# Optimization experiments

Measured on AMD Instinct MI355X. Metric: run time of the kernel, lower is better.

Reference implementation:

```python
import jax, jax.numpy as jnp
import numpy as np

D_MODEL = 1024
N_HEADS = 16
N_KV = 1          # MQA: the torch module only repeats xk_attn/sv, so n_kv must be 1 or n_heads
HEAD_DIM = 64     # d_model // total_n_heads
B = 1
L = 2048
SCALE = 1.0 / np.sqrt(HEAD_DIM)


def _rope(x, cos, sin):
    # x: [B, L, H, hd]; cos/sin: [L, hd//2]; pairs are consecutive elements (llama2.c style)
    xr, xi = x[..., 0::2], x[..., 1::2]
    c = cos[None, :, None, :]
    s = sin[None, :, None, :]
    out_r = xr * c - xi * s
    out_i = xr * s + xi * c
    return jnp.stack([out_r, out_i], axis=-1).reshape(x.shape)


def setup_inputs() -> dict:
    key = jax.random.key(0)
    ks = jax.random.split(key, 8)
    x = jax.random.normal(ks[0], (B, L, D_MODEL), dtype=jnp.float32)
    symbols = jax.random.normal(ks[1], (B, L, D_MODEL), dtype=jnp.float32)
    # standard RoPE frequencies
    inv_freq = 1.0 / (10000.0 ** (np.arange(0, HEAD_DIM, 2, dtype=np.float64) / HEAD_DIM))
    angles = np.outer(np.arange(L, dtype=np.float64), inv_freq)
    freqs_cos = jnp.asarray(np.cos(angles), dtype=jnp.float32)
    freqs_sin = jnp.asarray(np.sin(angles), dtype=jnp.float32)
    s = 0.02
    wq_attn = jax.random.normal(ks[2], (D_MODEL, N_HEADS * HEAD_DIM), dtype=jnp.float32) * s
    wk_attn = jax.random.normal(ks[3], (D_MODEL, N_KV * HEAD_DIM), dtype=jnp.float32) * s
    wq_rel = jax.random.normal(ks[4], (D_MODEL, N_HEADS * HEAD_DIM), dtype=jnp.float32) * s
    wk_rel = jax.random.normal(ks[5], (D_MODEL, N_KV * HEAD_DIM), dtype=jnp.float32) * s
    wv = jax.random.normal(ks[6], (D_MODEL, N_KV * HEAD_DIM), dtype=jnp.float32) * s
    wo = jax.random.normal(ks[7], (N_HEADS * HEAD_DIM, N_HEADS * HEAD_DIM), dtype=jnp.float32) * s
    return {"x": x, "symbols": symbols, "freqs_cos": freqs_cos, "freqs_sin": freqs_sin,
            "wq_attn": wq_attn, "wk_attn": wk_attn, "wq_rel": wq_rel, "wk_rel": wk_rel,
            "wv": wv, "wo": wo}


def reference(x, symbols, freqs_cos, freqs_sin, wq_attn, wk_attn, wq_rel, wk_rel, wv, wo):
    bsz, seqlen, _ = x.shape
    n_rep = N_HEADS // N_KV
    # projections
    xq_a = (x @ wq_attn).reshape(bsz, seqlen, N_HEADS, HEAD_DIM)
    xk_a = (x @ wk_attn).reshape(bsz, seqlen, N_KV, HEAD_DIM)
    xq_r = (x @ wq_rel).reshape(bsz, seqlen, N_HEADS, HEAD_DIM)
    xk_r = (x @ wk_rel).reshape(bsz, seqlen, N_KV, HEAD_DIM)
    sv = (symbols @ wv).reshape(bsz, seqlen, N_KV, HEAD_DIM)
    # RoPE only on attention q/k (matches torch code)
    xq_a = _rope(xq_a, freqs_cos, freqs_sin)
    xk_a = _rope(xk_a, freqs_cos, freqs_sin)
    # GQA/MQA head repetition of attn keys and symbol-values (NOT rel keys, per source)
    xk_a = jnp.repeat(xk_a, n_rep, axis=2)   # [B, L, H, hd]
    sv = jnp.repeat(sv, n_rep, axis=2)       # [B, L, H, hd]
    # attention scores with causal mask
    attn_scores = jnp.einsum('bihd,bjhd->bhij', xq_a, xk_a) * SCALE
    causal_bias = jnp.where(jnp.tril(jnp.ones((seqlen, seqlen), dtype=bool)),
                            jnp.float32(0.0), -jnp.inf)
    attn_scores = jax.nn.softmax(attn_scores + causal_bias, axis=-1)
    # relation scores: xk_r has N_KV=1 heads, broadcast against H query heads (identity activation)
    rel_scores = jnp.einsum('bihd,bjd->bhij', xq_r, xk_r[:, :, 0, :]) * SCALE
    rca_scores = attn_scores * rel_scores
    out = jnp.einsum('bhij,bjhd->bihd', rca_scores, sv)
    out = out.reshape(bsz, seqlen, N_HEADS * HEAD_DIM) @ wo
    return (out, attn_scores, rel_scores)
```

## Files before the change

kernel.cpp:

```cpp
#include <hip/hip_runtime.h>
#include <hip/hip_bf16.h>
#include <stdint.h>

#define LQ 2048
#define DM 1024
#define NH 16
#define HD 64
#define NPAIR 32
#define SCALE_F 0.125f

#define QROWS 16
__global__ __launch_bounds__(256) void k_proj_q(
    const float* __restrict__ x, const float* __restrict__ wqa, const float* __restrict__ wqr,
    const float* __restrict__ fcos, const float* __restrict__ fsin,
    float* __restrict__ Qa, float* __restrict__ Qr)
{
    __shared__ float xS[QROWS * DM];
    const int bid = blockIdx.x;
    const int i0 = (bid >> 2) * QROWS;
    const int m = (bid >> 1) & 1;
    const int half = bid & 1;
    const int tid = threadIdx.x;
    {
        const float4* src = (const float4*)(x + (size_t)i0 * DM);
        float4* dst4 = (float4*)xS;
        for (int t = tid; t < QROWS * DM / 4; t += 256) dst4[t] = src[t];
    }
    __syncthreads();
    const int q = half * 256 + tid;
    const float2* __restrict__ w2 = (const float2*)(m ? wqr : wqa);
    float ae[QROWS], ao[QROWS];
#pragma unroll
    for (int r = 0; r < QROWS; ++r) { ae[r] = 0.f; ao[r] = 0.f; }
    for (int k = 0; k < DM; k += 4) {
        float2 w0 = w2[(size_t)(k + 0) * (DM / 2) + q];
        float2 w1 = w2[(size_t)(k + 1) * (DM / 2) + q];
        float2 w2v = w2[(size_t)(k + 2) * (DM / 2) + q];
        float2 w3 = w2[(size_t)(k + 3) * (DM / 2) + q];
#pragma unroll
        for (int r = 0; r < QROWS; ++r) {
            float4 xv = *(const float4*)&xS[r * DM + k];
            ae[r] = fmaf(xv.x, w0.x, ae[r]);  ao[r] = fmaf(xv.x, w0.y, ao[r]);
            ae[r] = fmaf(xv.y, w1.x, ae[r]);  ao[r] = fmaf(xv.y, w1.y, ao[r]);
            ae[r] = fmaf(xv.z, w2v.x, ae[r]); ao[r] = fmaf(xv.z, w2v.y, ao[r]);
            ae[r] = fmaf(xv.w, w3.x, ae[r]);  ao[r] = fmaf(xv.w, w3.y, ao[r]);
        }
    }
    float* __restrict__ dst = m ? Qr : Qa;
    const int p = q & (NPAIR - 1);
#pragma unroll
    for (int r = 0; r < QROWS; ++r) {
        float oe = ae[r], oo = ao[r];
        if (m == 0) {
            float c = fcos[(i0 + r) * NPAIR + p];
            float s = fsin[(i0 + r) * NPAIR + p];
            oe = ae[r] * c - ao[r] * s;
            oo = ae[r] * s + ao[r] * c;
        }
        *(float2*)&dst[(size_t)(i0 + r) * DM + 2 * q] = make_float2(oe, oo);
    }
}

#define KVROWS 8
__global__ __launch_bounds__(128) void k_proj_kv(
    const float* __restrict__ x, const float* __restrict__ symbols,
    const float* __restrict__ wka, const float* __restrict__ wkr, const float* __restrict__ wv,
    const float* __restrict__ fcos, const float* __restrict__ fsin,
    float* __restrict__ Ka, float* __restrict__ Kr, float* __restrict__ SV)
{
    __shared__ float xS[KVROWS * DM], sS[KVROWS * DM];
    const int i0 = blockIdx.x * KVROWS;
    const int tid = threadIdx.x;
    {
        const float4* sx = (const float4*)(x + (size_t)i0 * DM);
        const float4* ss = (const float4*)(symbols + (size_t)i0 * DM);
        for (int t = tid; t < KVROWS * DM / 4; t += 128) {
            ((float4*)xS)[t] = sx[t];
            ((float4*)sS)[t] = ss[t];
        }
    }
    __syncthreads();
    if (tid >= 96) return;
    const int m = tid >> 5;
    const int p = tid & 31;
    const float2* __restrict__ w2 = (const float2*)(m == 0 ? wka : (m == 1 ? wkr : wv));
    const float* __restrict__ src = (m == 2) ? sS : xS;
    float ae[KVROWS], ao[KVROWS];
#pragma unroll
    for (int r = 0; r < KVROWS; ++r) { ae[r] = 0.f; ao[r] = 0.f; }
    for (int k = 0; k < DM; ++k) {
        float2 w = w2[k * 32 + p];
#pragma unroll
        for (int r = 0; r < KVROWS; ++r) {
            float xv = src[r * DM + k];
            ae[r] = fmaf(xv, w.x, ae[r]);
            ao[r] = fmaf(xv, w.y, ao[r]);
        }
    }
    float* __restrict__ dst = (m == 0 ? Ka : (m == 1 ? Kr : SV));
#pragma unroll
    for (int r = 0; r < KVROWS; ++r) {
        float oe = ae[r], oo = ao[r];
        if (m == 0) {
            float c = fcos[(i0 + r) * NPAIR + p];
            float s = fsin[(i0 + r) * NPAIR + p];
            oe = ae[r] * c - ao[r] * s;
            oo = ae[r] * s + ao[r] * c;
        }
        dst[(i0 + r) * HD + 2 * p] = oe;
        dst[(i0 + r) * HD + 2 * p + 1] = oo;
    }
}

__global__ __launch_bounds__(256) void k_rel(
    const float* __restrict__ Qr, const float* __restrict__ Kr, float* __restrict__ relout)
{
    __shared__ float QS[128 * 68];
    __shared__ float KS[64 * 68];
    const int j0 = blockIdx.x * 64, i0 = blockIdx.y * 128, h = blockIdx.z;
    const int tid = threadIdx.x;
    for (int t = tid; t < 128 * 16; t += 256) {
        int r = t >> 4, c4 = (t & 15) << 2;
        *(float4*)&QS[r * 68 + c4] = *(const float4*)&Qr[(size_t)(i0 + r) * DM + h * HD + c4];
    }
    for (int t = tid; t < 64 * 16; t += 256) {
        int r = t >> 4, c4 = (t & 15) << 2;
        *(float4*)&KS[r * 68 + c4] = *(const float4*)&Kr[(j0 + r) * HD + c4];
    }
    __syncthreads();
    const int ti = tid & 15, tj = tid >> 4;
    float acc[8][4] = {};
#pragma unroll 2
    for (int d = 0; d < HD; d += 4) {
        float4 kv[4];
#pragma unroll
        for (int b = 0; b < 4; ++b) kv[b] = *(const float4*)&KS[(tj * 4 + b) * 68 + d];
#pragma unroll
        for (int a = 0; a < 8; ++a) {
            float4 qv = *(const float4*)&QS[(ti + 16 * a) * 68 + d];
#pragma unroll
            for (int b = 0; b < 4; ++b) {
                acc[a][b] = fmaf(qv.x, kv[b].x, acc[a][b]);
                acc[a][b] = fmaf(qv.y, kv[b].y, acc[a][b]);
                acc[a][b] = fmaf(qv.z, kv[b].z, acc[a][b]);
                acc[a][b] = fmaf(qv.w, kv[b].w, acc[a][b]);
            }
        }
    }
#pragma unroll
    for (int a = 0; a < 8; ++a) {
        float4 w = make_float4(acc[a][0] * SCALE_F, acc[a][1] * SCALE_F,
                               acc[a][2] * SCALE_F, acc[a][3] * SCALE_F);
        *(float4*)&relout[(size_t)(h * LQ + i0 + ti + 16 * a) * LQ + j0 + tj * 4] = w;
    }
}

__global__ __launch_bounds__(256) void k_attn_fused(
    const float* __restrict__ Qa, const float* __restrict__ Ka, const float* __restrict__ SV,
    const float* __restrict__ relin, float* __restrict__ attnout, float* __restrict__ OutH)
{
    __shared__ float QS[64 * 68];
    __shared__ float KSbuf[64 * 68];
    __shared__ float SVS[64 * 68];
    const int bid = blockIdx.x;
    const int h = bid & 15;
    const int m = bid >> 4;
    const int it = (m < 16) ? m : 47 - m;
    const int i0 = it * 64;
    const int tid = threadIdx.x;
    for (int t = tid; t < 64 * 16; t += 256) {
        int r = t >> 4, c4 = (t & 15) << 2;
        *(float4*)&QS[r * 68 + c4] = *(const float4*)&Qa[(size_t)(i0 + r) * DM + h * HD + c4];
    }
    const int ti = tid & 15, tj = tid >> 4;
    float l_[4] = {0.f, 0.f, 0.f, 0.f};
    float oacc[4][4] = {};
    float* pS = KSbuf;
    for (int jt = 0; jt <= it; ++jt) {
        const int j0 = jt * 64;
        __syncthreads();
        for (int t = tid; t < 64 * 16; t += 256) {
            int r = t >> 4, c4 = (t & 15) << 2;
            *(float4*)&KSbuf[r * 68 + c4] = *(const float4*)&Ka[(j0 + r) * HD + c4];
            *(float4*)&SVS[r * 68 + c4]  = *(const float4*)&SV[(j0 + r) * HD + c4];
        }
        const int jb = j0 + tj * 4;
        float4 rv[4];
#pragma unroll
        for (int a = 0; a < 4; ++a)
            rv[a] = *(const float4*)&relin[(size_t)(h * LQ + i0 + ti + 16 * a) * LQ + jb];
        __syncthreads();
        float s[4][4] = {};
#pragma unroll 2
        for (int d = 0; d < HD; d += 4) {
            float4 kv[4];
#pragma unroll
            for (int b = 0; b < 4; ++b) kv[b] = *(const float4*)&KSbuf[(tj * 4 + b) * 68 + d];
#pragma unroll
            for (int a = 0; a < 4; ++a) {
                float4 qv = *(const float4*)&QS[(ti + 16 * a) * 68 + d];
#pragma unroll
                for (int b = 0; b < 4; ++b) {
                    s[a][b] = fmaf(qv.x, kv[b].x, s[a][b]);
                    s[a][b] = fmaf(qv.y, kv[b].y, s[a][b]);
                    s[a][b] = fmaf(qv.z, kv[b].z, s[a][b]);
                    s[a][b] = fmaf(qv.w, kv[b].w, s[a][b]);
                }
            }
        }
        __syncthreads();
#pragma unroll
        for (int a = 0; a < 4; ++a) {
            const int i = i0 + ti + 16 * a;
            const float* rl = (const float*)&rv[a];
            float e0 = (jb + 0 <= i) ? __expf(s[a][0] * SCALE_F) : 0.f;
            float e1 = (jb + 1 <= i) ? __expf(s[a][1] * SCALE_F) : 0.f;
            float e2 = (jb + 2 <= i) ? __expf(s[a][2] * SCALE_F) : 0.f;
            float e3 = (jb + 3 <= i) ? __expf(s[a][3] * SCALE_F) : 0.f;
            l_[a] += e0 + e1 + e2 + e3;
            *(float4*)&pS[(ti + 16 * a) * 68 + tj * 4] =
                make_float4(e0 * rl[0], e1 * rl[1], e2 * rl[2], e3 * rl[3]);
            *(float4*)&attnout[(size_t)(h * LQ + i) * LQ + jb] =
                make_float4(e0, e1, e2, e3);
        }
        __syncthreads();
#pragma unroll 2
        for (int g = 0; g < 64; g += 4) {
            float4 sv0 = *(const float4*)&SVS[(g + 0) * 68 + tj * 4];
            float4 sv1 = *(const float4*)&SVS[(g + 1) * 68 + tj * 4];
            float4 sv2 = *(const float4*)&SVS[(g + 2) * 68 + tj * 4];
            float4 sv3 = *(const float4*)&SVS[(g + 3) * 68 + tj * 4];
#pragma unroll
            for (int a = 0; a < 4; ++a) {
                float4 p4 = *(const float4*)&pS[(ti + 16 * a) * 68 + g];
                oacc[a][0] = fmaf(p4.x, sv0.x, oacc[a][0]);
                oacc[a][1] = fmaf(p4.x, sv0.y, oacc[a][1]);
                oacc[a][2] = fmaf(p4.x, sv0.z, oacc[a][2]);
                oacc[a][3] = fmaf(p4.x, sv0.w, oacc[a][3]);
                oacc[a][0] = fmaf(p4.y, sv1.x, oacc[a][0]);
                oacc[a][1] = fmaf(p4.y, sv1.y, oacc[a][1]);
                oacc[a][2] = fmaf(p4.y, sv1.z, oacc[a][2]);
                oacc[a][3] = fmaf(p4.y, sv1.w, oacc[a][3]);
                oacc[a][0] = fmaf(p4.z, sv2.x, oacc[a][0]);
                oacc[a][1] = fmaf(p4.z, sv2.y, oacc[a][1]);
                oacc[a][2] = fmaf(p4.z, sv2.z, oacc[a][2]);
                oacc[a][3] = fmaf(p4.z, sv2.w, oacc[a][3]);
                oacc[a][0] = fmaf(p4.w, sv3.x, oacc[a][0]);
                oacc[a][1] = fmaf(p4.w, sv3.y, oacc[a][1]);
                oacc[a][2] = fmaf(p4.w, sv3.z, oacc[a][2]);
                oacc[a][3] = fmaf(p4.w, sv3.w, oacc[a][3]);
            }
        }
    }
    __syncthreads();
    float* red = SVS;
#pragma unroll
    for (int a = 0; a < 4; ++a) red[(ti + 16 * a) * 17 + tj] = l_[a];
    __syncthreads();
    if (tid < 64) {
        float Ls = 0.f;
#pragma unroll
        for (int t = 0; t < 16; ++t) Ls += red[tid * 17 + t];
        red[tid * 17 + 16] = 1.0f / Ls;
    }
    __syncthreads();
#pragma unroll
    for (int a = 0; a < 4; ++a) {
        float inv = red[(ti + 16 * a) * 17 + 16];
        *(float4*)&OutH[(size_t)(i0 + ti + 16 * a) * DM + h * HD + tj * 4] =
            make_float4(oacc[a][0] * inv, oacc[a][1] * inv,
                        oacc[a][2] * inv, oacc[a][3] * inv);
    }
    const int lastc4 = (it + 1) * 16;
    for (int idx = tid; idx < 64 * (LQ / 4); idx += 256) {
        const int r = idx >> 9, c4 = idx & 511;
        float* p = &attnout[(size_t)(h * LQ + i0 + r) * LQ + (c4 << 2)];
        if (c4 < lastc4) {
            const float inv = red[r * 17 + 16];
            float4 v = *(const float4*)p;
            v.x *= inv; v.y *= inv; v.z *= inv; v.w *= inv;
            *(float4*)p = v;
        } else {
            *(float4*)p = make_float4(0.f, 0.f, 0.f, 0.f);
        }
    }
}

__global__ __launch_bounds__(256) void k_outproj(
    const float* __restrict__ OutH, const float* __restrict__ wo, float* __restrict__ outp)
{
    __shared__ float AS[64 * 68];
    __shared__ float BS[64 * 68];
    const int n0 = blockIdx.x * 64, i0 = blockIdx.y * 64;
    const int tid = threadIdx.x;
    const int ti = tid & 15, tj = tid >> 4;
    float acc[4][4] = {};
    for (int kt = 0; kt < DM / 64; ++kt) {
        const int k0 = kt * 64;
        __syncthreads();
        for (int t = tid; t < 64 * 16; t += 256) {
            int r = t >> 4, c4 = (t & 15) << 2;
            *(float4*)&AS[r * 68 + c4] = *(const float4*)&OutH[(size_t)(i0 + r) * DM + k0 + c4];
            *(float4*)&BS[r * 68 + c4] = *(const float4*)&wo[(size_t)(k0 + r) * DM + n0 + c4];
        }
        __syncthreads();
#pragma unroll 2
        for (int kk = 0; kk < 64; kk += 4) {
            float4 b0 = *(const float4*)&BS[(kk + 0) * 68 + tj * 4];
            float4 b1 = *(const float4*)&BS[(kk + 1) * 68 + tj * 4];
            float4 b2 = *(const float4*)&BS[(kk + 2) * 68 + tj * 4];
            float4 b3 = *(const float4*)&BS[(kk + 3) * 68 + tj * 4];
#pragma unroll
            for (int a = 0; a < 4; ++a) {
                float4 av = *(const float4*)&AS[(ti + 16 * a) * 68 + kk];
                acc[a][0] = fmaf(av.x, b0.x, acc[a][0]); acc[a][1] = fmaf(av.x, b0.y, acc[a][1]);
                acc[a][2] = fmaf(av.x, b0.z, acc[a][2]); acc[a][3] = fmaf(av.x, b0.w, acc[a][3]);
                acc[a][0] = fmaf(av.y, b1.x, acc[a][0]); acc[a][1] = fmaf(av.y, b1.y, acc[a][1]);
                acc[a][2] = fmaf(av.y, b1.z, acc[a][2]); acc[a][3] = fmaf(av.y, b1.w, acc[a][3]);
                acc[a][0] = fmaf(av.z, b2.x, acc[a][0]); acc[a][1] = fmaf(av.z, b2.y, acc[a][1]);
                acc[a][2] = fmaf(av.z, b2.z, acc[a][2]); acc[a][3] = fmaf(av.z, b2.w, acc[a][3]);
                acc[a][0] = fmaf(av.w, b3.x, acc[a][0]); acc[a][1] = fmaf(av.w, b3.y, acc[a][1]);
                acc[a][2] = fmaf(av.w, b3.z, acc[a][2]); acc[a][3] = fmaf(av.w, b3.w, acc[a][3]);
            }
        }
    }
#pragma unroll
    for (int a = 0; a < 4; ++a) {
        *(float4*)&outp[(size_t)(i0 + ti + 16 * a) * DM + n0 + tj * 4] =
            make_float4(acc[a][0], acc[a][1], acc[a][2], acc[a][3]);
    }
}

extern "C" void kernel_launch(void* const* d_in, const int* in_sizes, int n_in,
                              void* d_out, int out_size, void* d_ws, size_t ws_size,
                              hipStream_t stream)
{
    const float* x       = (const float*)d_in[0];
    const float* symbols = (const float*)d_in[1];
    const float* fcos    = (const float*)d_in[2];
    const float* fsin    = (const float*)d_in[3];
    const float* wqa     = (const float*)d_in[4];
    const float* wka     = (const float*)d_in[5];
    const float* wqr     = (const float*)d_in[6];
    const float* wkr     = (const float*)d_in[7];
    const float* wv      = (const float*)d_in[8];
    const float* wo      = (const float*)d_in[9];

    float* out_main = (float*)d_out;
    float* out_attn = out_main + (size_t)LQ * DM;
    float* out_rel  = out_attn + (size_t)NH * LQ * LQ;

    float* ws   = (float*)d_ws;
    float* Qa   = ws;
    float* Qr   = Qa + (size_t)LQ * DM;
    float* Ka   = Qr + (size_t)LQ * DM;
    float* Kr   = Ka + (size_t)LQ * HD;
    float* SV   = Kr + (size_t)LQ * HD;
    float* Mrow = SV + (size_t)LQ * HD;
    float* Lrow = Mrow + (size_t)NH * LQ;
    float* OutH = Lrow + (size_t)NH * LQ;

    k_proj_q<<<dim3((LQ / QROWS) * 4), 256, 0, stream>>>(x, wqa, wqr, fcos, fsin, Qa, Qr);
    k_proj_kv<<<dim3(LQ / KVROWS), 128, 0, stream>>>(x, symbols, wka, wkr, wv, fcos, fsin, Ka, Kr, SV);
    k_rel<<<dim3(32, 16, 16), 256, 0, stream>>>(Qr, Kr, out_rel);
    k_attn_fused<<<dim3(32 * 16), 256, 0, stream>>>(Qa, Ka, SV, out_rel, out_attn, OutH);
    k_outproj<<<dim3(16, 32), 256, 0, stream>>>(OutH, wo, out_main);
}
```

Before: 1.263 ms.

## Double-buffer K/SV tiles with register prefetch and XOR-swizzled shared memory

The fused attention kernel now prefetches the next K and SV tiles into registers while computing the current tile, then writes them into an alternate shared buffer. Shared arrays switch from padded stride-68 rows to an XOR swizzle to avoid bank conflicts, and the launch bounds request two blocks per CU. The aim is to hide global load latency and cut LDS conflicts. In exchange it uses more shared memory (five 16KB buffers) and more registers for the prefetch, which may limit occupancy.

```diff
diff --git a/kernel.cpp b/kernel.cpp
--- a/kernel.cpp
+++ b/kernel.cpp
@@ -8,6 +8,8 @@
 #define HD 64
 #define NPAIR 32
 #define SCALE_F 0.125f
+
+#define SWZ(row, ch) (((row) << 6) + ((((ch) ^ ((row) & 15))) << 2))
 
 #define QROWS 16
 __global__ __launch_bounds__(256) void k_proj_q(
@@ -155,50 +157,64 @@
     }
 }
 
-__global__ __launch_bounds__(256) void k_attn_fused(
+__global__ __launch_bounds__(256, 2) void k_attn_fused(
     const float* __restrict__ Qa, const float* __restrict__ Ka, const float* __restrict__ SV,
     const float* __restrict__ relin, float* __restrict__ attnout, float* __restrict__ OutH)
 {
-    __shared__ float QS[64 * 68];
-    __shared__ float KSbuf[64 * 68];
-    __shared__ float SVS[64 * 68];
+    __shared__ float QS[4096];
+    __shared__ float Kbuf[2][4096];
+    __shared__ float SVbuf[2][4096];
     const int bid = blockIdx.x;
     const int h = bid & 15;
     const int m = bid >> 4;
     const int it = (m < 16) ? m : 47 - m;
     const int i0 = it * 64;
     const int tid = threadIdx.x;
-    for (int t = tid; t < 64 * 16; t += 256) {
-        int r = t >> 4, c4 = (t & 15) << 2;
-        *(float4*)&QS[r * 68 + c4] = *(const float4*)&Qa[(size_t)(i0 + r) * DM + h * HD + c4];
-    }
     const int ti = tid & 15, tj = tid >> 4;
+
+#pragma unroll
+    for (int c = 0; c < 4; ++c) {
+        int t = tid + c * 256;
+        int r = t >> 4, cc = t & 15;
+        *(float4*)&QS[SWZ(r, cc)] =
+            *(const float4*)&Qa[(size_t)(i0 + r) * DM + h * HD + (cc << 2)];
+        *(float4*)&Kbuf[0][SWZ(r, cc)]  = *(const float4*)&Ka[(size_t)r * HD + (cc << 2)];
+        *(float4*)&SVbuf[0][SWZ(r, cc)] = *(const float4*)&SV[(size_t)r * HD + (cc << 2)];
+    }
+    __syncthreads();
+
     float l_[4] = {0.f, 0.f, 0.f, 0.f};
     float oacc[4][4] = {};
-    float* pS = KSbuf;
     for (int jt = 0; jt <= it; ++jt) {
-        const int j0 = jt * 64;
-        __syncthreads();
-        for (int t = tid; t < 64 * 16; t += 256) {
-            int r = t >> 4, c4 = (t & 15) << 2;
-            *(float4*)&KSbuf[r * 68 + c4] = *(const float4*)&Ka[(j0 + r) * HD + c4];
-            *(float4*)&SVS[r * 68 + c4]  = *(const float4*)&SV[(j0 + r) * HD + c4];
+        const int cur = jt & 1;
+        const int j0 = jt << 6;
+        float4 pk[4], psv[4];
+        if (jt < it) {
+            const int j0n = j0 + 64;
+#pragma unroll
+            for (int c = 0; c < 4; ++c) {
+                int t = tid + c * 256;
+                int r = t >> 4, cc = t & 15;
+                pk[c]  = *(const float4*)&Ka[(size_t)(j0n + r) * HD + (cc << 2)];
+                psv[c] = *(const float4*)&SV[(size_t)(j0n + r) * HD + (cc << 2)];
+            }
         }
         const int jb = j0 + tj * 4;
         float4 rv[4];
 #pragma unroll
         for (int a = 0; a < 4; ++a)
             rv[a] = *(const float4*)&relin[(size_t)(h * LQ + i0 + ti + 16 * a) * LQ + jb];
-        __syncthreads();
+        const float* Kc = Kbuf[cur];
         float s[4][4] = {};
 #pragma unroll 2
         for (int d = 0; d < HD; d += 4) {
+            const int dc = d >> 2;
             float4 kv[4];
 #pragma unroll
-            for (int b = 0; b < 4; ++b) kv[b] = *(const float4*)&KSbuf[(tj * 4 + b) * 68 + d];
+            for (int b = 0; b < 4; ++b) kv[b] = *(const float4*)&Kc[SWZ(tj * 4 + b, dc)];
 #pragma unroll
             for (int a = 0; a < 4; ++a) {
-                float4 qv = *(const float4*)&QS[(ti + 16 * a) * 68 + d];
+                float4 qv = *(const float4*)&QS[SWZ(ti + 16 * a, dc)];
 #pragma unroll
                 for (int b = 0; b < 4; ++b) {
                     s[a][b] = fmaf(qv.x, kv[b].x, s[a][b]);
@@ -209,6 +225,18 @@
             }
         }
         __syncthreads();
+        if (jt < it) {
+            float* Kn = Kbuf[cur ^ 1];
+            float* Sn = SVbuf[cur ^ 1];
+#pragma unroll
+            for (int c = 0; c < 4; ++c) {
+                int t = tid + c * 256;
+                int r = t >> 4, cc = t & 15;
+                *(float4*)&Kn[SWZ(r, cc)] = pk[c];
+                *(float4*)&Sn[SWZ(r, cc)] = psv[c];
+            }
+        }
+        float* Pc = Kbuf[cur];
 #pragma unroll
         for (int a = 0; a < 4; ++a) {
             const int i = i0 + ti + 16 * a;
@@ -218,21 +246,22 @@
             float e2 = (jb + 2 <= i) ? __expf(s[a][2] * SCALE_F) : 0.f;
             float e3 = (jb + 3 <= i) ? __expf(s[a][3] * SCALE_F) : 0.f;
             l_[a] += e0 + e1 + e2 + e3;
-            *(float4*)&pS[(ti + 16 * a) * 68 + tj * 4] =
+            *(float4*)&Pc[SWZ(ti + 16 * a, tj)] =
                 make_float4(e0 * rl[0], e1 * rl[1], e2 * rl[2], e3 * rl[3]);
             *(float4*)&attnout[(size_t)(h * LQ + i) * LQ + jb] =
                 make_float4(e0, e1, e2, e3);
         }
         __syncthreads();
+        const float* SVc = SVbuf[cur];
 #pragma unroll 2
         for (int g = 0; g < 64; g += 4) {
-            float4 sv0 = *(const float4*)&SVS[(g + 0) * 68 + tj * 4];
-            float4 sv1 = *(const float4*)&SVS[(g + 1) * 68 + tj * 4];
-            float4 sv2 = *(const float4*)&SVS[(g + 2) * 68 + tj * 4];
-            float4 sv3 = *(const float4*)&SVS[(g + 3) * 68 + tj * 4];
+            float4 sv0 = *(const float4*)&SVc[SWZ(g + 0, tj)];
+            float4 sv1 = *(const float4*)&SVc[SWZ(g + 1, tj)];
+            float4 sv2 = *(const float4*)&SVc[SWZ(g + 2, tj)];
+            float4 sv3 = *(const float4*)&SVc[SWZ(g + 3, tj)];
 #pragma unroll
             for (int a = 0; a < 4; ++a) {
-                float4 p4 = *(const float4*)&pS[(ti + 16 * a) * 68 + g];
+                float4 p4 = *(const float4*)&Pc[SWZ(ti + 16 * a, g >> 2)];
                 oacc[a][0] = fmaf(p4.x, sv0.x, oacc[a][0]);
                 oacc[a][1] = fmaf(p4.x, sv0.y, oacc[a][1]);
                 oacc[a][2] = fmaf(p4.x, sv0.z, oacc[a][2]);
@@ -251,9 +280,9 @@
                 oacc[a][3] = fmaf(p4.w, sv3.w, oacc[a][3]);
             }
         }
-    }
-    __syncthreads();
-    float* red = SVS;
+        __syncthreads();
+    }
+    float* red = QS;
 #pragma unroll
     for (int a = 0; a < 4; ++a) red[(ti + 16 * a) * 17 + tj] = l_[a];
     __syncthreads();
```

Result: no change. 1.268 ms (+0.4%).
